# Kernel optimization log

Measured on AMD Instinct MI355X. Metric: run time of the kernel, lower is better.

The kernel has to match this reference:

```python
import jax, jax.numpy as jnp
import numpy as np

B, S, H, P2 = 64, 512, 768, 46  # batch, seq, hidden, num_p*2


def setup_inputs() -> dict:
    key = jax.random.key(0)
    k1, k2, k3, k4 = jax.random.split(key, 4)
    hidden_states = jax.random.normal(k1, (B, S, H), dtype=jnp.float32)
    # subject start/end indices must lie within the valid (masked-in) prefix
    lengths = jax.random.randint(k2, (B,), S // 4, S + 1)  # cue lengths per sample
    input_mask = (jnp.arange(S)[None, :] < lengths[:, None]).astype(jnp.int32)
    ids = jax.random.randint(k3, (B, 2), 0, S // 4)
    batch_subject_ids = jnp.sort(ids, axis=1).astype(jnp.int32)
    W = jax.random.normal(k4, (P2, H), dtype=jnp.float32) * (1.0 / np.sqrt(H))
    b = jnp.zeros((P2,), dtype=jnp.float32)
    return {"hidden_states": hidden_states, "batch_subject_ids": batch_subject_ids,
            "input_mask": input_mask, "W": W, "b": b}


def reference(hidden_states, batch_subject_ids, input_mask, W, b):
    # per-sample subject embedding: h[b, start] + h[b, end]  -> [B, H]
    batch_idx = jnp.arange(hidden_states.shape[0])
    s = (hidden_states[batch_idx, batch_subject_ids[:, 0]]
         + hidden_states[batch_idx, batch_subject_ids[:, 1]])
    # broadcast-add s to the first cue_len positions of each sample
    cue_len = jnp.sum(input_mask, axis=1)  # [B]
    pos_mask = (jnp.arange(hidden_states.shape[1])[None, :] < cue_len[:, None])  # [B, S]
    h = hidden_states + s[:, None, :] * pos_mask[:, :, None].astype(hidden_states.dtype)
    # linear + sigmoid^4 (dropout is identity in eval mode)
    logits = jnp.einsum('bsh,ph->bsp', h, W) + b
    return jax.nn.sigmoid(logits) ** 4
```

## Files before the change

kernel.cpp:

```cpp
#include <hip/hip_runtime.h>

#define SEQ 512
#define HID 768
#define P2  46
#define MT  64
#define KC  64
#define BLK 512
#define NCHUNK (HID / KC)

typedef short bf16x8 __attribute__((ext_vector_type(8)));
typedef float f32x4  __attribute__((ext_vector_type(4)));

__device__ __forceinline__ unsigned short f2bf(float f) {
  union { float f; unsigned int u; } v; v.f = f;
  return (unsigned short)((v.u + 0x7FFFu + ((v.u >> 16) & 1u)) >> 16);
}

__device__ __forceinline__ void async_ld16(const void* g, void* l) {
  __builtin_amdgcn_global_load_lds(
      (const __attribute__((address_space(1))) unsigned int*)g,
      (__attribute__((address_space(3))) unsigned int*)l, 16, 0, 0);
}

__global__ __launch_bounds__(BLK, 4) void fused_kernel(
    const float* __restrict__ h, const int* __restrict__ ids,
    const int* __restrict__ mask, const float* __restrict__ W,
    const float* __restrict__ bias, float* __restrict__ out) {

  __shared__ __align__(16) unsigned char  hA[2][16 * 1088];
  __shared__ __align__(16) unsigned short wB[2][48][64];
  __shared__ float q_s[P2];

  const int tid  = threadIdx.x;
  const int lane = tid & 63, wv = tid >> 6;
  const int mr = lane & 15, qd = lane >> 4;
  const int wm = wv >> 1, wn = wv & 1;
  const int row0 = blockIdx.x * MT;
  const int b    = row0 >> 9;

  auto stageH = [&](int c, int buf) {
    #pragma unroll
    for (int j2 = 0; j2 < 2; ++j2) {
      int j = (wv << 1) + j2;
      int r = (j << 2) + (lane >> 4);
      int gc = ((lane >> 1) & 7) ^ (r & 7);
      const float* src = h + (size_t)(row0 + r) * HID + (c << 6)
                           + (gc << 3) + ((lane & 1) << 2);
      async_ld16(src, &hA[buf][j * 1088]);
    }
  };

  auto stageW = [&](int c, int buf) {
    #pragma unroll
    for (int i = 0; i < 2; ++i) {
      int idx = tid + (i << 9);
      if (idx < 768) {
        int r = idx >> 4, c4 = idx & 15;
        float4 v = (r < P2)
            ? *(const float4*)(W + (size_t)r * HID + (c << 6) + (c4 << 2))
            : make_float4(0.f, 0.f, 0.f, 0.f);
        ushort4 u;
        u.x = f2bf(v.x); u.y = f2bf(v.y); u.z = f2bf(v.z); u.w = f2bf(v.w);
        int dst = (((c4 >> 1) ^ (r & 7)) << 3) + ((c4 & 1) << 2);
        *(ushort4*)&wB[buf][r][dst] = u;
      }
    }
  };

  f32x4 acc[2];
  acc[0] = f32x4{0.f, 0.f, 0.f, 0.f};
  acc[1] = f32x4{0.f, 0.f, 0.f, 0.f};

  auto compute = [&](int buf) {
    #pragma unroll
    for (int ks = 0; ks < 2; ++ks) {
      int r  = (wm << 4) + mr;
      int cp = ((ks << 2) + qd) ^ (r & 7);
      const float4* ap =
          (const float4*)&hA[buf][(r >> 2) * 1088 + ((r & 3) << 8) + (cp << 5)];
      float4 a0 = ap[0], a1 = ap[1];
      bf16x8 a = { (short)f2bf(a0.x), (short)f2bf(a0.y),
                   (short)f2bf(a0.z), (short)f2bf(a0.w),
                   (short)f2bf(a1.x), (short)f2bf(a1.y),
                   (short)f2bf(a1.z), (short)f2bf(a1.w) };
      int bswz = (((ks << 2) + qd) ^ (mr & 7)) << 3;
      {
        int p = (wn << 5) + mr;
        bf16x8 bb = *(const bf16x8*)&wB[buf][p][bswz];
        acc[0] = __builtin_amdgcn_mfma_f32_16x16x32_bf16(a, bb, acc[0], 0, 0, 0);
      }
      if (!wn) {
        bf16x8 bb = *(const bf16x8*)&wB[buf][16 + mr][bswz];
        acc[1] = __builtin_amdgcn_mfma_f32_16x16x32_bf16(a, bb, acc[1], 0, 0, 0);
      }
    }
  };

  stageH(0, 0);
  stageW(0, 0);

  {
    const int i0 = ids[b * 2 + 0], i1 = ids[b * 2 + 1];
    const float* r0p = h + ((size_t)b * SEQ + i0) * HID;
    const float* r1p = h + ((size_t)b * SEQ + i1) * HID;
    for (int p = wv; p < P2; p += 8) {
      const float* wp = W + (size_t)p * HID;
      float a = 0.f;
      #pragma unroll
      for (int j = 0; j < HID / 64; ++j) {
        int k = lane + (j << 6);
        a += (r0p[k] + r1p[k]) * wp[k];
      }
      #pragma unroll
      for (int off = 32; off > 0; off >>= 1) a += __shfl_xor(a, off, 64);
      if (lane == 0) q_s[p] = a;
    }
  }
  __syncthreads();

  for (int c = 0; c < NCHUNK; ++c) {
    int buf = c & 1;
    if (c + 1 < NCHUNK) { stageH(c + 1, buf ^ 1); stageW(c + 1, buf ^ 1); }
    compute(buf);
    __syncthreads();
  }

  const int rbase = row0 + (wm << 4) + (qd << 2);
  int msk[4];
  #pragma unroll
  for (int i = 0; i < 4; ++i) msk[i] = mask[rbase + i];

  auto storeNT = [&](f32x4 a, int p) {
    if (p < P2) {
      float bv = bias[p], qv = q_s[p];
      #pragma unroll
      for (int i = 0; i < 4; ++i) {
        float x = a[i] + bv + (msk[i] ? qv : 0.f);
        float sg = 1.f / (1.f + __expf(-x));
        sg *= sg; sg *= sg;
        out[(size_t)(rbase + i) * P2 + p] = sg;
      }
    }
  };
  storeNT(acc[0], (wn << 5) + mr);
  if (!wn) storeNT(acc[1], 16 + mr);
}

extern "C" void kernel_launch(void* const* d_in, const int* in_sizes, int n_in,
                              void* d_out, int out_size, void* d_ws, size_t ws_size,
                              hipStream_t stream) {
  const float* h    = (const float*)d_in[0];
  const int*   ids  = (const int*)d_in[1];
  const int*   mask = (const int*)d_in[2];
  const float* W    = (const float*)d_in[3];
  const float* bias = (const float*)d_in[4];
  float* out = (float*)d_out;

  fused_kernel<<<dim3((64 * SEQ) / MT), BLK, 0, stream>>>(h, ids, mask, W, bias, out);
}
```

Measured before the change: 163.9 us.

## Stage all of W in LDS once and stream activations through registers

The per-chunk double-buffered LDS staging of both activations and weights is replaced. The full bf16 weight matrix is now converted into LDS once per block, and each wave streams its own 16 activation rows directly from global memory into registers with a 4-deep software prefetch. The K loop runs with no barriers, and each wave computes all three 16-column output tiles with 256-thread blocks. This removes the per-chunk __syncthreads and repeated W staging. In exchange it uses a larger LDS footprint, which limits occupancy to 2 blocks, and relies on register-level latency hiding for uncoalesced-ish row loads. Padding rows 46-47 of the weights are left uninitialised, but they only feed output columns that are never stored.

```diff
diff --git a/kernel.cpp b/kernel.cpp
--- a/kernel.cpp
+++ b/kernel.cpp
@@ -4,9 +4,9 @@
 #define HID 768
 #define P2  46
 #define MT  64
-#define KC  64
-#define BLK 512
-#define NCHUNK (HID / KC)
+#define BLK 256
+#define NSTEP (HID / 32)
+#define WROWS 48
 
 typedef short bf16x8 __attribute__((ext_vector_type(8)));
 typedef float f32x4  __attribute__((ext_vector_type(4)));
@@ -16,94 +16,40 @@
   return (unsigned short)((v.u + 0x7FFFu + ((v.u >> 16) & 1u)) >> 16);
 }
 
-__device__ __forceinline__ void async_ld16(const void* g, void* l) {
-  __builtin_amdgcn_global_load_lds(
-      (const __attribute__((address_space(1))) unsigned int*)g,
-      (__attribute__((address_space(3))) unsigned int*)l, 16, 0, 0);
-}
-
-__global__ __launch_bounds__(BLK, 4) void fused_kernel(
+__global__ __launch_bounds__(BLK, 2) void fused_kernel(
     const float* __restrict__ h, const int* __restrict__ ids,
     const int* __restrict__ mask, const float* __restrict__ W,
     const float* __restrict__ bias, float* __restrict__ out) {
 
-  __shared__ __align__(16) unsigned char  hA[2][16 * 1088];
-  __shared__ __align__(16) unsigned short wB[2][48][64];
+  __shared__ __align__(16) unsigned short wB[WROWS][HID];
   __shared__ float q_s[P2];
 
   const int tid  = threadIdx.x;
   const int lane = tid & 63, wv = tid >> 6;
   const int mr = lane & 15, qd = lane >> 4;
-  const int wm = wv >> 1, wn = wv & 1;
   const int row0 = blockIdx.x * MT;
   const int b    = row0 >> 9;
 
-  auto stageH = [&](int c, int buf) {
-    #pragma unroll
-    for (int j2 = 0; j2 < 2; ++j2) {
-      int j = (wv << 1) + j2;
-      int r = (j << 2) + (lane >> 4);
-      int gc = ((lane >> 1) & 7) ^ (r & 7);
-      const float* src = h + (size_t)(row0 + r) * HID + (c << 6)
-                           + (gc << 3) + ((lane & 1) << 2);
-      async_ld16(src, &hA[buf][j * 1088]);
+  #pragma unroll
+  for (int i = 0; i < 35; ++i) {
+    int idx = tid + i * BLK;
+    if (idx < P2 * 192) {
+      int p  = idx / 192;
+      int c4 = idx - p * 192;
+      float4 v = *(const float4*)(W + (size_t)p * HID + (c4 << 2));
+      ushort4 u;
+      u.x = f2bf(v.x); u.y = f2bf(v.y); u.z = f2bf(v.z); u.w = f2bf(v.w);
+      int c  = c4 >> 1;
+      int cs = (c & 0x78) | ((c ^ p) & 7);
+      *(ushort4*)&wB[p][(cs << 3) + ((c4 & 1) << 2)] = u;
     }
-  };
-
-  auto stageW = [&](int c, int buf) {
-    #pragma unroll
-    for (int i = 0; i < 2; ++i) {
-      int idx = tid + (i << 9);
-      if (idx < 768) {
-        int r = idx >> 4, c4 = idx & 15;
-        float4 v = (r < P2)
-            ? *(const float4*)(W + (size_t)r * HID + (c << 6) + (c4 << 2))
-            : make_float4(0.f, 0.f, 0.f, 0.f);
-        ushort4 u;
-        u.x = f2bf(v.x); u.y = f2bf(v.y); u.z = f2bf(v.z); u.w = f2bf(v.w);
-        int dst = (((c4 >> 1) ^ (r & 7)) << 3) + ((c4 & 1) << 2);
-        *(ushort4*)&wB[buf][r][dst] = u;
-      }
-    }
-  };
-
-  f32x4 acc[2];
-  acc[0] = f32x4{0.f, 0.f, 0.f, 0.f};
-  acc[1] = f32x4{0.f, 0.f, 0.f, 0.f};
-
-  auto compute = [&](int buf) {
-    #pragma unroll
-    for (int ks = 0; ks < 2; ++ks) {
-      int r  = (wm << 4) + mr;
-      int cp = ((ks << 2) + qd) ^ (r & 7);
-      const float4* ap =
-          (const float4*)&hA[buf][(r >> 2) * 1088 + ((r & 3) << 8) + (cp << 5)];
-      float4 a0 = ap[0], a1 = ap[1];
-      bf16x8 a = { (short)f2bf(a0.x), (short)f2bf(a0.y),
-                   (short)f2bf(a0.z), (short)f2bf(a0.w),
-                   (short)f2bf(a1.x), (short)f2bf(a1.y),
-                   (short)f2bf(a1.z), (short)f2bf(a1.w) };
-      int bswz = (((ks << 2) + qd) ^ (mr & 7)) << 3;
-      {
-        int p = (wn << 5) + mr;
-        bf16x8 bb = *(const bf16x8*)&wB[buf][p][bswz];
-        acc[0] = __builtin_amdgcn_mfma_f32_16x16x32_bf16(a, bb, acc[0], 0, 0, 0);
-      }
-      if (!wn) {
-        bf16x8 bb = *(const bf16x8*)&wB[buf][16 + mr][bswz];
-        acc[1] = __builtin_amdgcn_mfma_f32_16x16x32_bf16(a, bb, acc[1], 0, 0, 0);
-      }
-    }
-  };
-
-  stageH(0, 0);
-  stageW(0, 0);
+  }
 
   {
     const int i0 = ids[b * 2 + 0], i1 = ids[b * 2 + 1];
     const float* r0p = h + ((size_t)b * SEQ + i0) * HID;
     const float* r1p = h + ((size_t)b * SEQ + i1) * HID;
-    for (int p = wv; p < P2; p += 8) {
+    for (int p = wv; p < P2; p += 4) {
       const float* wp = W + (size_t)p * HID;
       float a = 0.f;
       #pragma unroll
@@ -116,34 +62,61 @@
       if (lane == 0) q_s[p] = a;
     }
   }
+
+  const int arow = row0 + (wv << 4) + mr;
+  const float* abase = h + (size_t)arow * HID + (qd << 3);
+  float4 pa[4][2];
+  #pragma unroll
+  for (int s = 0; s < 4; ++s) {
+    pa[s][0] = *(const float4*)(abase + (s << 5));
+    pa[s][1] = *(const float4*)(abase + (s << 5) + 4);
+  }
+
   __syncthreads();
 
-  for (int c = 0; c < NCHUNK; ++c) {
-    int buf = c & 1;
-    if (c + 1 < NCHUNK) { stageH(c + 1, buf ^ 1); stageW(c + 1, buf ^ 1); }
-    compute(buf);
-    __syncthreads();
+  f32x4 acc[3];
+  #pragma unroll
+  for (int nt = 0; nt < 3; ++nt) acc[nt] = f32x4{0.f, 0.f, 0.f, 0.f};
+
+  #pragma unroll
+  for (int s = 0; s < NSTEP; ++s) {
+    float4 c0 = pa[s & 3][0], c1 = pa[s & 3][1];
+    if (s + 4 < NSTEP) {
+      pa[s & 3][0] = *(const float4*)(abase + ((s + 4) << 5));
+      pa[s & 3][1] = *(const float4*)(abase + ((s + 4) << 5) + 4);
+    }
+    bf16x8 a = { (short)f2bf(c0.x), (short)f2bf(c0.y),
+                 (short)f2bf(c0.z), (short)f2bf(c0.w),
+                 (short)f2bf(c1.x), (short)f2bf(c1.y),
+                 (short)f2bf(c1.z), (short)f2bf(c1.w) };
+    int c  = (s << 2) + qd;
+    int cs = (c & 0x78) | ((c ^ mr) & 7);
+    #pragma unroll
+    for (int nt = 0; nt < 3; ++nt) {
+      bf16x8 bb = *(const bf16x8*)&wB[(nt << 4) + mr][cs << 3];
+      acc[nt] = __builtin_amdgcn_mfma_f32_16x16x32_bf16(a, bb, acc[nt], 0, 0, 0);
+    }
   }
 
-  const int rbase = row0 + (wm << 4) + (qd << 2);
+  const int rbase = row0 + (wv << 4) + (qd << 2);
   int msk[4];
   #pragma unroll
   for (int i = 0; i < 4; ++i) msk[i] = mask[rbase + i];
 
-  auto storeNT = [&](f32x4 a, int p) {
+  #pragma unroll
+  for (int nt = 0; nt < 3; ++nt) {
+    int p = (nt << 4) + mr;
     if (p < P2) {
       float bv = bias[p], qv = q_s[p];
       #pragma unroll
       for (int i = 0; i < 4; ++i) {
-        float x = a[i] + bv + (msk[i] ? qv : 0.f);
+        float x = acc[nt][i] + bv + (msk[i] ? qv : 0.f);
         float sg = 1.f / (1.f + __expf(-x));
         sg *= sg; sg *= sg;
         out[(size_t)(rbase + i) * P2 + p] = sg;
       }
     }
-  };
-  storeNT(acc[0], (wn << 5) + mr);
-  if (!wn) storeNT(acc[1], 16 + mr);
+  }
 }
 
 extern "C" void kernel_launch(void* const* d_in, const int* in_sizes, int n_in,
```

New measurement: 166.6 us. About the same (+1.7%).
